# Kernel optimization log

Hardware: AMD Instinct MI355X
Metric: run time of the kernel (lower is better)

## Reference

```python
import jax, jax.numpy as jnp
import numpy as np

BS, NS, NCP, NH, C, HID, R = 8, 2048, 8, 8, 128, 128, 128


def rotation_6d_to_matrix(d6):
    a1, a2 = d6[..., :3], d6[..., 3:]
    b1 = a1 / jnp.linalg.norm(a1, axis=-1, keepdims=True)
    b2 = a2 - jnp.sum(b1 * a2, axis=-1, keepdims=True) * b1
    b2 = b2 / jnp.linalg.norm(b2, axis=-1, keepdims=True)
    b3 = jnp.cross(b1, b2)
    return jnp.stack([b1, b2, b3], axis=-2)  # (..., 3, 3), rows b1,b2,b3


def _sample_plane(plane, uv):
    # plane: (B,C,R,R); uv: (B,N,2) in [0,1]; uv[...,0]->width, uv[...,1]->height
    Rr = plane.shape[-1]
    x = jnp.clip(uv[..., 0], 0.0, 1.0) * (Rr - 1)
    y = jnp.clip(uv[..., 1], 0.0, 1.0) * (Rr - 1)
    x0 = jnp.floor(x); y0 = jnp.floor(y)
    wx = x - x0; wy = y - y0
    x0i = x0.astype(jnp.int32); y0i = y0.astype(jnp.int32)
    x1i = jnp.minimum(x0i + 1, Rr - 1); y1i = jnp.minimum(y0i + 1, Rr - 1)
    gb = jax.vmap(lambda p, yi, xi: p[:, yi, xi])  # per-batch gather -> (C,N)
    f00 = gb(plane, y0i, x0i); f01 = gb(plane, y0i, x1i)
    f10 = gb(plane, y1i, x0i); f11 = gb(plane, y1i, x1i)
    wx = wx[:, None, :]; wy = wy[:, None, :]
    f = f00 * (1 - wx) * (1 - wy) + f01 * wx * (1 - wy) + f10 * (1 - wx) * wy + f11 * wx * wy
    return jnp.transpose(f, (0, 2, 1))  # (B,N,C)


def triplane_sample(p, pxz, pxy, pyz):
    # p: (B,N,3) in [0,1]^3; sum of bilinear samples from the three planes
    return (_sample_plane(pxz, p[..., jnp.array([0, 2])])
            + _sample_plane(pxy, p[..., jnp.array([0, 1])])
            + _sample_plane(pyz, p[..., jnp.array([1, 2])]))


def setup_inputs() -> dict:
    key = jax.random.key(0)
    ks = jax.random.split(key, 10)
    s = 1.0 / np.sqrt(C)
    return {
        "query_pos": jax.random.uniform(ks[0], (BS, NS, 9), dtype=jnp.float32),
        "plane_xz": jax.random.normal(ks[1], (BS, C, R, R), dtype=jnp.float32),
        "plane_xy": jax.random.normal(ks[2], (BS, C, R, R), dtype=jnp.float32),
        "plane_yz": jax.random.normal(ks[3], (BS, C, R, R), dtype=jnp.float32),
        "control_points": jax.random.normal(ks[4], (NCP, 3), dtype=jnp.float32) * 0.05,
        "W_v": jax.random.normal(ks[5], (C, HID), dtype=jnp.float32) * s,
        "b_v": jnp.zeros((HID,), jnp.float32),
        "W_w": jax.random.normal(ks[6], (C, NCP * NH), dtype=jnp.float32) * s,
        "b_w": jnp.zeros((NCP * NH,), jnp.float32),
        "W_o": jax.random.normal(ks[7], (HID, C), dtype=jnp.float32) * s,
        "b_o": jnp.zeros((C,), jnp.float32),
    }


def reference(query_pos, plane_xz, plane_xy, plane_yz, control_points,
              W_v, b_v, W_w, b_w, W_o, b_o):
    bs, ns, _ = query_pos.shape
    q_ori = query_pos[..., 3:]
    q_pos = query_pos[..., :3]
    feature = triplane_sample(q_pos, plane_xz, plane_xy, plane_yz)  # (bs,ns,C)
    rot = rotation_6d_to_matrix(q_ori)  # (bs,ns,3,3)
    # rotate control points: einsum('bnpd,bngd->bngp') with cp broadcast over (bs,ns)
    cp = jnp.einsum('bnpd,gd->bngp', rot, control_points)  # (bs,ns,ncp,3)
    anchor = q_pos[:, :, None, :] + cp  # (bs,ns,ncp,3)
    sf = triplane_sample(anchor.reshape(bs, ns * NCP, 3), plane_xz, plane_xy, plane_yz)
    sf = sf.reshape(bs * ns, NCP, C)  # head dim in torch code is a pure repeat
    feat = feature.reshape(bs * ns, C)
    w = (feat @ W_w + b_w).reshape(bs * ns, NCP, NH)  # (B,ncp,heads)
    vbase = sf @ W_v + b_v  # (B,ncp,hid); identical across repeated head dim
    # torch: (v * weights).sum((1,2)) with v_t[b,i,j,k]=vbase[b,j,k], w[b,i,j]
    out = jnp.einsum('bjk,bij->bk', vbase, w)  # (B,hid)
    out = out @ W_o + b_o
    out = out + feat
    return out.reshape(bs, ns, -1)
```

## Files before the change

### kernel.cpp

```cpp
#include <hip/hip_runtime.h>
#include <hip/hip_fp16.h>
#include <math.h>

constexpr int BS  = 8;
constexpr int NS  = 2048;
constexpr int NCP = 8;
constexpr int NH  = 8;
constexpr int C   = 128;
constexpr int HID = 128;
constexpr int RR  = 128;

constexpr int QPB = 8;
constexpr int VEC = 4;

constexpr int NPOS = RR * RR;
constexpr size_t PLE = (size_t)BS * NPOS * C;

constexpr int TPOS   = 64;
constexpr int NBLK_T = 3 * BS * (NPOS / TPOS);
constexpr int LDSP   = 132;

struct F4 { float x, y, z, w; };
__device__ __forceinline__ F4 f4add(F4 a, F4 b) {
    return F4{a.x + b.x, a.y + b.y, a.z + b.z, a.w + b.w};
}
__device__ __forceinline__ F4 f4fma(F4 acc, float s, F4 v) {
    return F4{fmaf(s, v.x, acc.x), fmaf(s, v.y, acc.y),
              fmaf(s, v.z, acc.z), fmaf(s, v.w, acc.w)};
}
__device__ __forceinline__ F4 cvt4(int2 r) {
    __half2 h0 = *reinterpret_cast<__half2*>(&r.x);
    __half2 h1 = *reinterpret_cast<__half2*>(&r.y);
    float2 f0 = __half22float2(h0);
    float2 f1 = __half22float2(h1);
    return F4{f0.x, f0.y, f1.x, f1.y};
}

__global__ __launch_bounds__(256) void trans_prep_k(
    const float* __restrict__ pxz, const float* __restrict__ pxy,
    const float* __restrict__ pyz, __half* __restrict__ dst,
    const float* __restrict__ Wv, const float* __restrict__ bv,
    const float* __restrict__ Ww, const float* __restrict__ bw,
    const float* __restrict__ Wo,
    float* __restrict__ Wf, float* __restrict__ bf,
    float* __restrict__ Ww2, float* __restrict__ bw2)
{
    const int bid = blockIdx.x;
    const int t   = threadIdx.x;

    if (bid >= NBLK_T) {
        const int k = bid - NBLK_T;
        const int c = t;
        if (c >= 128) return;
        if (k < 128) {
            float acc = 0.f;
            #pragma unroll 8
            for (int j = 0; j < 128; ++j) acc += Wv[k * 128 + j] * Wo[j * 128 + c];
            Wf[k * 128 + c] = acc;
        } else if (k == 128) {
            float acc = 0.f;
            #pragma unroll 8
            for (int j = 0; j < 128; ++j) acc += bv[j] * Wo[j * 128 + c];
            bf[c] = acc;
        } else {
            float s[NH];
            #pragma unroll
            for (int h = 0; h < NH; ++h) s[h] = 0.f;
            #pragma unroll
            for (int i = 0; i < NCP; ++i)
                #pragma unroll
                for (int h = 0; h < NH; ++h) s[h] += Ww[c * (NCP * NH) + i * NH + h];
            #pragma unroll
            for (int h = 0; h < NH; ++h) Ww2[c * NH + h] = s[h];
            if (c < NH) {
                float tt = 0.f;
                #pragma unroll
                for (int i = 0; i < NCP; ++i) tt += bw[i * NH + c];
                bw2[c] = tt;
            }
        }
        return;
    }

    const int b   = bid & 7;
    const int idx = bid >> 3;
    const int pl  = idx >> 8;
    const int n0  = (idx & 255) * TPOS;

    const float* src = (pl == 0 ? pxz : (pl == 1 ? pxy : pyz))
                       + (size_t)b * C * NPOS;
    __half* d = dst + (size_t)(pl * BS + b) * ((size_t)NPOS * C);

    __shared__ __half lds[TPOS * LDSP];

    #pragma unroll
    for (int i = 0; i < 8; ++i) {
        int li = i * 256 + t;
        int m  = li >> 4;
        int k4 = (li & 15) << 2;
        float4 v = *reinterpret_cast<const float4*>(src + (size_t)m * NPOS + n0 + k4);
        lds[(k4 + 0) * LDSP + m] = __float2half(v.x);
        lds[(k4 + 1) * LDSP + m] = __float2half(v.y);
        lds[(k4 + 2) * LDSP + m] = __float2half(v.z);
        lds[(k4 + 3) * LDSP + m] = __float2half(v.w);
    }
    __syncthreads();

    #pragma unroll
    for (int i = 0; i < 8; ++i) {
        int li = i * 256 + t;
        int n  = li >> 5;
        int c4 = (li & 31) << 2;
        uint2 v = *reinterpret_cast<const uint2*>(lds + n * LDSP + c4);
        *reinterpret_cast<uint2*>(d + (size_t)(n0 + n) * C + c4) = v;
    }
}

__device__ __forceinline__ F4 samp(const __half* __restrict__ base, float u, float v)
{
    float x = fminf(fmaxf(u, 0.f), 1.f) * (float)(RR - 1);
    float y = fminf(fmaxf(v, 0.f), 1.f) * (float)(RR - 1);
    float x0f = floorf(x), y0f = floorf(y);
    float wx = x - x0f, wy = y - y0f;
    int x0 = (int)x0f, y0 = (int)y0f;
    int x1 = min(x0 + 1, RR - 1), y1 = min(y0 + 1, RR - 1);
    int r0 = y0 << 14, r1 = y1 << 14, cc0 = x0 << 7, cc1 = x1 << 7;
    int2 a00 = *reinterpret_cast<const int2*>(base + r0 + cc0);
    int2 a01 = *reinterpret_cast<const int2*>(base + r0 + cc1);
    int2 a10 = *reinterpret_cast<const int2*>(base + r1 + cc0);
    int2 a11 = *reinterpret_cast<const int2*>(base + r1 + cc1);
    float w00 = (1.f - wx) * (1.f - wy), w01 = wx * (1.f - wy);
    float w10 = (1.f - wx) * wy,         w11 = wx * wy;
    F4 f00 = cvt4(a00), f01 = cvt4(a01), f10 = cvt4(a10), f11 = cvt4(a11);
    F4 r;
    r.x = f00.x * w00 + f01.x * w01 + f10.x * w10 + f11.x * w11;
    r.y = f00.y * w00 + f01.y * w01 + f10.y * w10 + f11.y * w11;
    r.z = f00.z * w00 + f01.z * w01 + f10.z * w10 + f11.z * w11;
    r.w = f00.w * w00 + f01.w * w01 + f10.w * w10 + f11.w * w11;
    return r;
}

__global__ __launch_bounds__(256) void attn_k(
    const float* __restrict__ qpos,
    const __half* __restrict__ planes,
    const float* __restrict__ cpts,
    const float* __restrict__ Ww2, const float* __restrict__ bw2,
    const float* __restrict__ Wf,  const float* __restrict__ bf,
    const float* __restrict__ bo,
    float* __restrict__ out)
{
    const int nb   = gridDim.x;
    const int cpx  = nb >> 3;
    const int sbid = (blockIdx.x & 7) * cpx + (blockIdx.x >> 3);

    const int tid  = threadIdx.x;
    const int ql   = tid >> 5;
    const int lane = tid & 31;
    const int c4   = lane * VEC;
    const int q    = sbid * QPB + ql;
    const int b    = q >> 11;

    const float* qp = qpos + (size_t)q * 9;
    const float px = qp[0], py = qp[1], pz = qp[2];
    const float a1x = qp[3], a1y = qp[4], a1z = qp[5];
    const float a2x = qp[6], a2y = qp[7], a2z = qp[8];

    float inv = 1.f / sqrtf(a1x * a1x + a1y * a1y + a1z * a1z);
    float b1x = a1x * inv, b1y = a1y * inv, b1z = a1z * inv;
    float dd  = b1x * a2x + b1y * a2y + b1z * a2z;
    float b2x = a2x - dd * b1x, b2y = a2y - dd * b1y, b2z = a2z - dd * b1z;
    inv = 1.f / sqrtf(b2x * b2x + b2y * b2y + b2z * b2z);
    b2x *= inv; b2y *= inv; b2z *= inv;
    float b3x = b1y * b2z - b1z * b2y;
    float b3y = b1z * b2x - b1x * b2z;
    float b3z = b1x * b2y - b1y * b2x;

    const __half* Pxz = planes + (size_t)b * ((size_t)NPOS * C) + c4;
    const __half* Pxy = Pxz + PLE;
    const __half* Pyz = Pxy + PLE;

    F4 feat = f4add(f4add(samp(Pxz, px, pz), samp(Pxy, px, py)), samp(Pyz, py, pz));

    float p[NH];
    #pragma unroll
    for (int h = 0; h < NH; ++h) p[h] = 0.f;
    {
        const float* wr = Ww2 + c4 * NH;
        const float fv[VEC] = {feat.x, feat.y, feat.z, feat.w};
        #pragma unroll
        for (int i = 0; i < VEC; ++i)
            #pragma unroll
            for (int h = 0; h < NH; ++h) p[h] += fv[i] * wr[i * NH + h];
    }
    #pragma unroll
    for (int off = 16; off >= 1; off >>= 1)
        #pragma unroll
        for (int h = 0; h < NH; ++h) p[h] += __shfl_xor(p[h], off);

    float ws[NH], Ssum = 0.f;
    #pragma unroll
    for (int h = 0; h < NH; ++h) { ws[h] = p[h] + bw2[h]; Ssum += ws[h]; }

    F4 comb = {0.f, 0.f, 0.f, 0.f};
    #pragma unroll 2
    for (int g = 0; g < NCP; ++g) {
        float cx = cpts[g * 3 + 0], cy = cpts[g * 3 + 1], cz = cpts[g * 3 + 2];
        float ax = px + b1x * cx + b1y * cy + b1z * cz;
        float ay = py + b2x * cx + b2y * cy + b2z * cz;
        float az = pz + b3x * cx + b3y * cy + b3z * cz;
        F4 s = f4add(f4add(samp(Pxz, ax, az), samp(Pxy, ax, ay)), samp(Pyz, ay, az));
        comb = f4fma(comb, ws[g], s);
    }

    __shared__ float sComb[QPB][C];
    __shared__ float sFeat[QPB][C];
    __shared__ float sSum[QPB];
    *reinterpret_cast<float4*>(&sComb[ql][c4]) = make_float4(comb.x, comb.y, comb.z, comb.w);
    *reinterpret_cast<float4*>(&sFeat[ql][c4]) = make_float4(feat.x, feat.y, feat.z, feat.w);
    if (lane == 0) sSum[ql] = Ssum;
    __syncthreads();

    const int c  = tid & 127;
    const int q0 = (tid >> 7) * 4;
    float acc[4];
    const float bfc = bf[c], boc = bo[c];
    #pragma unroll
    for (int j = 0; j < 4; ++j)
        acc[j] = sSum[q0 + j] * bfc + boc + sFeat[q0 + j][c];
    #pragma unroll 4
    for (int k = 0; k < C; ++k) {
        float wf = Wf[k * C + c];
        #pragma unroll
        for (int j = 0; j < 4; ++j) acc[j] += sComb[q0 + j][k] * wf;
    }
    #pragma unroll
    for (int j = 0; j < 4; ++j)
        out[(size_t)(sbid * QPB + q0 + j) * C + c] = acc[j];
}

extern "C" void kernel_launch(void* const* d_in, const int* in_sizes, int n_in,
                              void* d_out, int out_size, void* d_ws, size_t ws_size,
                              hipStream_t stream)
{
    const float* qpos = (const float*)d_in[0];
    const float* pxz  = (const float*)d_in[1];
    const float* pxy  = (const float*)d_in[2];
    const float* pyz  = (const float*)d_in[3];
    const float* cpts = (const float*)d_in[4];
    const float* Wv   = (const float*)d_in[5];
    const float* bv   = (const float*)d_in[6];
    const float* Ww   = (const float*)d_in[7];
    const float* bw   = (const float*)d_in[8];
    const float* Wo   = (const float*)d_in[9];
    const float* bo   = (const float*)d_in[10];
    float* out = (float*)d_out;

    __half* plh = (__half*)d_ws;
    float*  wsf = (float*)((char*)d_ws + 3 * PLE * sizeof(__half));
    float* Wf  = wsf;
    float* bf  = Wf + C * HID;
    float* Ww2 = bf + C;
    float* bw2 = Ww2 + C * NH;

    hipLaunchKernelGGL(trans_prep_k, dim3(NBLK_T + 130), dim3(256), 0, stream,
                       pxz, pxy, pyz, plh, Wv, bv, Ww, bw, Wo, Wf, bf, Ww2, bw2);

    hipLaunchKernelGGL(attn_k, dim3(BS * NS / QPB), dim3(256), 0, stream,
                       qpos, plh, cpts, Ww2, bw2, Wf, bf, bo, out);
}
```

Before: 121.2 us.

## Use direct global-to-LDS loads with XOR swizzle and permuted channel layout in transpose

```diff
diff --git a/kernel.cpp b/kernel.cpp
--- a/kernel.cpp
+++ b/kernel.cpp
@@ -18,7 +18,16 @@
 
 constexpr int TPOS   = 64;
 constexpr int NBLK_T = 3 * BS * (NPOS / TPOS);
-constexpr int LDSP   = 132;
+
+__host__ __device__ __forceinline__ int ch_of_slot(int s) {
+    return (s >> 3) + ((s & 7) << 4);
+}
+__host__ __device__ __forceinline__ int slot_of_ch(int c) {
+    return ((c & 15) << 3) | (c >> 4);
+}
+
+typedef __attribute__((address_space(3))) float lds_f;
+typedef const __attribute__((address_space(1))) float glb_f;
 
 struct F4 { float x, y, z, w; };
 __device__ __forceinline__ F4 f4add(F4 a, F4 b) {
@@ -53,9 +62,10 @@
         const int c = t;
         if (c >= 128) return;
         if (k < 128) {
+            const int kk = ch_of_slot(k);
             float acc = 0.f;
             #pragma unroll 8
-            for (int j = 0; j < 128; ++j) acc += Wv[k * 128 + j] * Wo[j * 128 + c];
+            for (int j = 0; j < 128; ++j) acc += Wv[kk * 128 + j] * Wo[j * 128 + c];
             Wf[k * 128 + c] = acc;
         } else if (k == 128) {
             float acc = 0.f;
@@ -63,13 +73,14 @@
             for (int j = 0; j < 128; ++j) acc += bv[j] * Wo[j * 128 + c];
             bf[c] = acc;
         } else {
+            const int cc = ch_of_slot(c);
             float s[NH];
             #pragma unroll
             for (int h = 0; h < NH; ++h) s[h] = 0.f;
             #pragma unroll
             for (int i = 0; i < NCP; ++i)
                 #pragma unroll
-                for (int h = 0; h < NH; ++h) s[h] += Ww[c * (NCP * NH) + i * NH + h];
+                for (int h = 0; h < NH; ++h) s[h] += Ww[cc * (NCP * NH) + i * NH + h];
             #pragma unroll
             for (int h = 0; h < NH; ++h) Ww2[c * NH + h] = s[h];
             if (c < NH) {
@@ -82,37 +93,50 @@
         return;
     }
 
-    const int b   = bid & 7;
-    const int idx = bid >> 3;
-    const int pl  = idx >> 8;
-    const int n0  = (idx & 255) * TPOS;
+    const int b    = bid & 7;
+    const int idx  = bid >> 3;
+    const int pl   = idx >> 8;
+    const int tile = idx & 255;
+    const int n0   = tile * TPOS;
 
     const float* src = (pl == 0 ? pxz : (pl == 1 ? pxy : pyz))
                        + (size_t)b * C * NPOS;
     __half* d = dst + (size_t)(pl * BS + b) * ((size_t)NPOS * C);
 
-    __shared__ __half lds[TPOS * LDSP];
-
-    #pragma unroll
-    for (int i = 0; i < 8; ++i) {
-        int li = i * 256 + t;
-        int m  = li >> 4;
-        int k4 = (li & 15) << 2;
-        float4 v = *reinterpret_cast<const float4*>(src + (size_t)m * NPOS + n0 + k4);
-        lds[(k4 + 0) * LDSP + m] = __float2half(v.x);
-        lds[(k4 + 1) * LDSP + m] = __float2half(v.y);
-        lds[(k4 + 2) * LDSP + m] = __float2half(v.z);
-        lds[(k4 + 3) * LDSP + m] = __float2half(v.w);
+    __shared__ float lds[C * TPOS];
+
+    const int wave = t >> 6;
+    const int lane = t & 63;
+    const int cw   = lane >> 4;
+    const int blk  = lane & 15;
+
+    #pragma unroll
+    for (int j = 0; j < 8; ++j) {
+        const int c0 = wave * 32 + j * 4;
+        const int c  = c0 + cw;
+        const int sb = blk ^ (c & 15);
+        glb_f* gp = (glb_f*)(src + (size_t)c * NPOS + n0 + sb * 4);
+        lds_f* lp = (lds_f*)(&lds[c0 * TPOS]);
+        __builtin_amdgcn_global_load_lds(gp, lp, 16, 0, 0);
     }
     __syncthreads();
 
     #pragma unroll
-    for (int i = 0; i < 8; ++i) {
-        int li = i * 256 + t;
-        int n  = li >> 5;
-        int c4 = (li & 31) << 2;
-        uint2 v = *reinterpret_cast<const uint2*>(lds + n * LDSP + c4);
-        *reinterpret_cast<uint2*>(d + (size_t)(n0 + n) * C + c4) = v;
+    for (int i = 0; i < 4; ++i) {
+        const int li = i * 256 + t;
+        const int n  = li >> 4;
+        const int g  = li & 15;
+        const int ro = (((n >> 2) ^ g) << 2) + (n & 3);
+        unsigned u[4];
+        #pragma unroll
+        for (int jj = 0; jj < 4; ++jj) {
+            const float vA = lds[(g + 32 * jj) * TPOS + ro];
+            const float vB = lds[(g + 32 * jj + 16) * TPOS + ro];
+            __half2 h = __floats2half2_rn(vA, vB);
+            u[jj] = *reinterpret_cast<unsigned*>(&h);
+        }
+        *reinterpret_cast<uint4*>(d + (size_t)(n0 + n) * C + g * 8) =
+            make_uint4(u[0], u[1], u[2], u[3]);
     }
 }
 
@@ -221,12 +245,13 @@
     __syncthreads();
 
     const int c  = tid & 127;
+    const int sl = slot_of_ch(c);
     const int q0 = (tid >> 7) * 4;
     float acc[4];
     const float bfc = bf[c], boc = bo[c];
     #pragma unroll
     for (int j = 0; j < 4; ++j)
-        acc[j] = sSum[q0 + j] * bfc + boc + sFeat[q0 + j][c];
+        acc[j] = sSum[q0 + j] * bfc + boc + sFeat[q0 + j][sl];
     #pragma unroll 4
     for (int k = 0; k < C; ++k) {
         float wf = Wf[k * C + c];
```

After: 120.2 us. No clear change (-0.8%).

## Restructure plane transpose into persistent channel-group blocks with software-pipelined loads

Applied to the files above, without the earlier changes.

```diff
diff --git a/kernel.cpp b/kernel.cpp
--- a/kernel.cpp
+++ b/kernel.cpp
@@ -16,9 +16,12 @@
 constexpr int NPOS = RR * RR;
 constexpr size_t PLE = (size_t)BS * NPOS * C;
 
-constexpr int TPOS   = 64;
-constexpr int NBLK_T = 3 * BS * (NPOS / TPOS);
-constexpr int LDSP   = 132;
+constexpr int NBLK_T = 768;
+constexpr int HPOS   = 8192;
+constexpr int SCPOS  = 1024;
+constexpr int LROW   = 1032;
+
+using f4v = __attribute__((ext_vector_type(4))) float;
 
 struct F4 { float x, y, z, w; };
 __device__ __forceinline__ F4 f4add(F4 a, F4 b) {
@@ -45,6 +48,8 @@
     float* __restrict__ Wf, float* __restrict__ bf,
     float* __restrict__ Ww2, float* __restrict__ bw2)
 {
+    __shared__ __half lh[8 * LROW];
+
     const int bid = blockIdx.x;
     const int t   = threadIdx.x;
 
@@ -82,37 +87,72 @@
         return;
     }
 
-    const int b   = bid & 7;
-    const int idx = bid >> 3;
-    const int pl  = idx >> 8;
-    const int n0  = (idx & 255) * TPOS;
-
-    const float* src = (pl == 0 ? pxz : (pl == 1 ? pxy : pyz))
-                       + (size_t)b * C * NPOS;
-    __half* d = dst + (size_t)(pl * BS + b) * ((size_t)NPOS * C);
-
-    __shared__ __half lds[TPOS * LDSP];
-
-    #pragma unroll
-    for (int i = 0; i < 8; ++i) {
-        int li = i * 256 + t;
-        int m  = li >> 4;
-        int k4 = (li & 15) << 2;
-        float4 v = *reinterpret_cast<const float4*>(src + (size_t)m * NPOS + n0 + k4);
-        lds[(k4 + 0) * LDSP + m] = __float2half(v.x);
-        lds[(k4 + 1) * LDSP + m] = __float2half(v.y);
-        lds[(k4 + 2) * LDSP + m] = __float2half(v.z);
-        lds[(k4 + 3) * LDSP + m] = __float2half(v.w);
-    }
-    __syncthreads();
-
-    #pragma unroll
-    for (int i = 0; i < 8; ++i) {
-        int li = i * 256 + t;
-        int n  = li >> 5;
-        int c4 = (li & 31) << 2;
-        uint2 v = *reinterpret_cast<const uint2*>(lds + n * LDSP + c4);
-        *reinterpret_cast<uint2*>(d + (size_t)(n0 + n) * C + c4) = v;
+    const int xcd = bid & 7;
+    const int rem = bid >> 3;
+    const int pl  = rem >> 5;
+    const int kk  = rem & 31;
+    const int hh  = kk >> 4;
+    const int g   = kk & 15;
+    const int b   = xcd;
+
+    const float* base = (pl == 0 ? pxz : (pl == 1 ? pxy : pyz));
+    const float* src = base + (size_t)b * C * NPOS + (size_t)(g * 8) * NPOS
+                            + (size_t)hh * HPOS;
+    __half* d = dst + (size_t)(pl * BS + b) * ((size_t)NPOS * C)
+                    + (size_t)hh * HPOS * C + g * 8;
+
+    const int cl  = t >> 5;
+    const int l32 = t & 31;
+
+    const float* sp0 = src + (size_t)cl * NPOS + l32 * 4;
+
+    f4v v[8];
+    #pragma unroll
+    for (int j = 0; j < 8; ++j)
+        v[j] = __builtin_nontemporal_load(
+                   reinterpret_cast<const f4v*>(sp0 + j * 128));
+
+    #pragma unroll
+    for (int sc = 0; sc < 8; ++sc) {
+        __syncthreads();
+
+        #pragma unroll
+        for (int j = 0; j < 8; ++j) {
+            __half2 h0 = __floats2half2_rn(v[j][0], v[j][1]);
+            __half2 h1 = __floats2half2_rn(v[j][2], v[j][3]);
+            uint2 w;
+            w.x = *reinterpret_cast<unsigned*>(&h0);
+            w.y = *reinterpret_cast<unsigned*>(&h1);
+            *reinterpret_cast<uint2*>(&lh[cl * LROW + l32 * 4 + j * 128]) = w;
+        }
+
+        f4v nv[8];
+        if (sc < 7) {
+            const float* sp = sp0 + (sc + 1) * SCPOS;
+            #pragma unroll
+            for (int j = 0; j < 8; ++j)
+                nv[j] = __builtin_nontemporal_load(
+                            reinterpret_cast<const f4v*>(sp + j * 128));
+        }
+        __syncthreads();
+
+        #pragma unroll
+        for (int i = 0; i < 4; ++i) {
+            const int p = t + i * 256;
+            unsigned short r[8];
+            #pragma unroll
+            for (int j = 0; j < 8; ++j)
+                r[j] = *reinterpret_cast<const unsigned short*>(&lh[j * LROW + p]);
+            uint4 u;
+            u.x = (unsigned)r[0] | ((unsigned)r[1] << 16);
+            u.y = (unsigned)r[2] | ((unsigned)r[3] << 16);
+            u.z = (unsigned)r[4] | ((unsigned)r[5] << 16);
+            u.w = (unsigned)r[6] | ((unsigned)r[7] << 16);
+            *reinterpret_cast<uint4*>(d + (size_t)(sc * SCPOS + p) * C) = u;
+        }
+
+        #pragma unroll
+        for (int j = 0; j < 8; ++j) v[j] = nv[j];
     }
 }
 
```

Measured after the change: 125.7 us. +3.7%, slower.

## Restructure plane transpose into persistent blocks with register-prefetched nontemporal loads

Applied to the files above, without the earlier changes.

```diff
diff --git a/kernel.cpp b/kernel.cpp
--- a/kernel.cpp
+++ b/kernel.cpp
@@ -16,9 +16,12 @@
 constexpr int NPOS = RR * RR;
 constexpr size_t PLE = (size_t)BS * NPOS * C;
 
-constexpr int TPOS   = 64;
-constexpr int NBLK_T = 3 * BS * (NPOS / TPOS);
-constexpr int LDSP   = 132;
+constexpr int NBLK_T = 384;
+constexpr int QPOS   = 2048;
+constexpr int SPOS   = 256;
+constexpr int LROWH  = 260;
+
+using f4v = __attribute__((ext_vector_type(4))) float;
 
 struct F4 { float x, y, z, w; };
 __device__ __forceinline__ F4 f4add(F4 a, F4 b) {
@@ -45,6 +48,8 @@
     float* __restrict__ Wf, float* __restrict__ bf,
     float* __restrict__ Ww2, float* __restrict__ bw2)
 {
+    __shared__ __half lh[64 * LROWH];
+
     const int bid = blockIdx.x;
     const int t   = threadIdx.x;
 
@@ -83,36 +88,80 @@
     }
 
     const int b   = bid & 7;
-    const int idx = bid >> 3;
-    const int pl  = idx >> 8;
-    const int n0  = (idx & 255) * TPOS;
+    const int rem = bid >> 3;
+    const int pl  = rem >> 4;
+    const int r2  = rem & 15;
+    const int cg  = r2 >> 3;
+    const int q   = r2 & 7;
+    const int ch0 = cg * 64;
+    const int pos0 = q * QPOS;
 
     const float* src = (pl == 0 ? pxz : (pl == 1 ? pxy : pyz))
                        + (size_t)b * C * NPOS;
     __half* d = dst + (size_t)(pl * BS + b) * ((size_t)NPOS * C);
 
-    __shared__ __half lds[TPOS * LDSP];
-
-    #pragma unroll
-    for (int i = 0; i < 8; ++i) {
-        int li = i * 256 + t;
-        int m  = li >> 4;
-        int k4 = (li & 15) << 2;
-        float4 v = *reinterpret_cast<const float4*>(src + (size_t)m * NPOS + n0 + k4);
-        lds[(k4 + 0) * LDSP + m] = __float2half(v.x);
-        lds[(k4 + 1) * LDSP + m] = __float2half(v.y);
-        lds[(k4 + 2) * LDSP + m] = __float2half(v.z);
-        lds[(k4 + 3) * LDSP + m] = __float2half(v.w);
-    }
-    __syncthreads();
-
-    #pragma unroll
-    for (int i = 0; i < 8; ++i) {
-        int li = i * 256 + t;
-        int n  = li >> 5;
-        int c4 = (li & 31) << 2;
-        uint2 v = *reinterpret_cast<const uint2*>(lds + n * LDSP + c4);
-        *reinterpret_cast<uint2*>(d + (size_t)(n0 + n) * C + c4) = v;
+    const int g32  = t >> 5;
+    const int l32  = t & 31;
+
+    f4v v[16];
+    #pragma unroll
+    for (int i = 0; i < 16; ++i) {
+        const int chL  = g32 * 8 + (i >> 1);
+        const int posL = ((i & 1) << 7) + (l32 << 2);
+        v[i] = __builtin_nontemporal_load(reinterpret_cast<const f4v*>(
+                   src + (size_t)(ch0 + chL) * NPOS + pos0 + posL));
+    }
+
+    #pragma unroll
+    for (int sc = 0; sc < 8; ++sc) {
+        __syncthreads();
+
+        #pragma unroll
+        for (int i = 0; i < 16; ++i) {
+            const int chL  = g32 * 8 + (i >> 1);
+            const int posL = ((i & 1) << 7) + (l32 << 2);
+            __half2 h0 = __floats2half2_rn(v[i][0], v[i][1]);
+            __half2 h1 = __floats2half2_rn(v[i][2], v[i][3]);
+            uint2 w;
+            w.x = *reinterpret_cast<unsigned*>(&h0);
+            w.y = *reinterpret_cast<unsigned*>(&h1);
+            *reinterpret_cast<uint2*>(&lh[chL * LROWH + posL]) = w;
+        }
+
+        f4v nv[16];
+        if (sc < 7) {
+            #pragma unroll
+            for (int i = 0; i < 16; ++i) {
+                const int chL  = g32 * 8 + (i >> 1);
+                const int posL = ((i & 1) << 7) + (l32 << 2);
+                nv[i] = __builtin_nontemporal_load(reinterpret_cast<const f4v*>(
+                            src + (size_t)(ch0 + chL) * NPOS + pos0
+                                + (sc + 1) * SPOS + posL));
+            }
+        }
+        __syncthreads();
+
+        {
+            const int p = t;
+            unsigned w[32];
+            #pragma unroll
+            for (int k = 0; k < 32; ++k) {
+                const unsigned lo = *reinterpret_cast<const unsigned short*>(
+                                        &lh[(2 * k) * LROWH + p]);
+                const unsigned hi = *reinterpret_cast<const unsigned short*>(
+                                        &lh[(2 * k + 1) * LROWH + p]);
+                w[k] = lo | (hi << 16);
+            }
+            __half* drow = d + (size_t)(pos0 + sc * SPOS + p) * C + ch0;
+            #pragma unroll
+            for (int j = 0; j < 8; ++j) {
+                *reinterpret_cast<uint4*>(drow + j * 8) =
+                    make_uint4(w[4 * j], w[4 * j + 1], w[4 * j + 2], w[4 * j + 3]);
+            }
+        }
+
+        #pragma unroll
+        for (int i = 0; i < 16; ++i) v[i] = nv[i];
     }
 }
 
```

Result: slower. 133.0 us (+9.7%).
